# Kernel tuning notes

Hardware: AMD Instinct MI355X
Metric: run time of the kernel (lower is better)

Reference implementation:

```python
import jax, jax.numpy as jnp
import numpy as np

# Transformer_E (depth=1): Residual(PreNorm(MultiScaleRetention)) + Residual1(PreNorm1(FeedForward))
# MultiScaleRetention follows the standard RetNet parallel form, adapted to two inputs
# (Q from x, K/V from z) as implied by PreNorm passing both normed streams to fn.

B, S, DIM, HEADS, MLP = 16, 1024, 256, 4, 512
HEAD = DIM // HEADS  # per-head qkv size; v_dim = DIM
EPS = 1e-5           # torch LayerNorm/GroupNorm default eps


def _ln(x, w, b):
    mu = jnp.mean(x, -1, keepdims=True)
    var = jnp.mean((x - mu) ** 2, -1, keepdims=True)
    return (x - mu) * jax.lax.rsqrt(var + EPS) * w + b


def _decay_matrix():
    # RetNet gammas: 1 - exp(linspace(log(1/32), log(1/512), heads))
    gammas = 1.0 - jnp.exp(jnp.linspace(jnp.log(1.0 / 32.0), jnp.log(1.0 / 512.0), HEADS))
    n = jnp.arange(S)
    diff = (n[:, None] - n[None, :]).astype(jnp.float32)  # [S,S]
    causal = diff >= 0
    D = jnp.where(causal[None], gammas[:, None, None] ** diff[None], 0.0)  # [H,S,S]
    return D.astype(jnp.float32)


def setup_inputs() -> dict:
    key = jax.random.key(0)
    ks = jax.random.split(key, 9)
    s = 1.0 / DIM  # repo inits W as randn/hidden_size
    return {
        "x": jax.random.normal(ks[0], (B, S, DIM), jnp.float32),
        "y": jax.random.normal(ks[1], (B, S, DIM), jnp.float32),
        "ln1_w": jnp.ones((DIM,), jnp.float32),
        "ln1_b": jnp.zeros((DIM,), jnp.float32),
        "W_Q": jax.random.normal(ks[2], (HEADS, DIM, HEAD), jnp.float32) * s,
        "W_K": jax.random.normal(ks[3], (HEADS, DIM, HEAD), jnp.float32) * s,
        "W_V": jax.random.normal(ks[4], (HEADS, DIM, HEAD), jnp.float32) * s,
        "gn_w": jnp.ones((DIM,), jnp.float32),
        "gn_b": jnp.zeros((DIM,), jnp.float32),
        "W_G": jax.random.normal(ks[5], (DIM, DIM), jnp.float32) * s,
        "W_O": jax.random.normal(ks[6], (DIM, DIM), jnp.float32) * s,
        "ln2_w": jnp.ones((DIM,), jnp.float32),
        "ln2_b": jnp.zeros((DIM,), jnp.float32),
        "ff_w1": jax.random.normal(ks[7], (DIM, MLP), jnp.float32) * (DIM ** -0.5),
        "ff_b1": jnp.zeros((MLP,), jnp.float32),
        "ff_w2": jax.random.normal(ks[8], (MLP, DIM), jnp.float32) * (MLP ** -0.5),
        "ff_b2": jnp.zeros((DIM,), jnp.float32),
    }


def reference(x, y, ln1_w, ln1_b, W_Q, W_K, W_V, gn_w, gn_b, W_G, W_O,
              ln2_w, ln2_b, ff_w1, ff_b1, ff_w2, ff_b2):
    # PreNorm: x.real -> float (already real float32 here), shared LayerNorm on both streams
    xn = _ln(x, ln1_w, ln1_b)
    zn = _ln(y, ln1_w, ln1_b)

    # --- MultiScaleRetention (parallel form) ---
    Q = jnp.einsum('bsd,hde->bhse', xn, W_Q)
    K = jnp.einsum('bsd,hde->bhse', zn, W_K)
    V = jnp.einsum('bsd,hde->bhse', zn, W_V)
    D = _decay_matrix()                                       # [H,S,S] causal decay
    scores = jnp.einsum('bhne,bhme->bhnm', Q, K) * D[None]    # [B,H,S,S]
    Yh = jnp.einsum('bhnm,bhme->bhne', scores, V)             # [B,H,S,HEAD]

    # GroupNorm(heads, v_dim) applied token-wise: normalize each head slice
    mu = jnp.mean(Yh, -1, keepdims=True)
    var = jnp.mean((Yh - mu) ** 2, -1, keepdims=True)
    Yn = (Yh - mu) * jax.lax.rsqrt(var + EPS)
    Ycat = jnp.transpose(Yn, (0, 2, 1, 3)).reshape(x.shape[0], x.shape[1], DIM)
    Ycat = Ycat * gn_w + gn_b

    # swish gate + output projection
    g = xn @ W_G
    attn_out = ((g * jax.nn.sigmoid(g)) * Ycat) @ W_O

    x1 = attn_out + x                                         # Residual

    # --- FeedForward block (Residual1(PreNorm1(FFN))) ---
    x1n = _ln(x1, ln2_w, ln2_b)
    h = jax.nn.leaky_relu(x1n @ ff_w1 + ff_b1, negative_slope=0.01)
    ff = h @ ff_w2 + ff_b2
    return ff + x1
```

## Files before the change

kernel.cpp:

```cpp
#include <hip/hip_runtime.h>

typedef float f32x4 __attribute__((ext_vector_type(4)));
typedef short bf16x8 __attribute__((ext_vector_type(8)));

__device__ __forceinline__ unsigned short f2bf(float f) {
  unsigned int u = __builtin_bit_cast(unsigned int, f);
  u += 0x7fffu + ((u >> 16) & 1u);
  return (unsigned short)(u >> 16);
}
__device__ __forceinline__ float bf2f(unsigned short s) {
  unsigned int u = ((unsigned int)s) << 16;
  return __builtin_bit_cast(float, u);
}

__device__ __forceinline__ void gll16(const void* src, void* dst) {
  __builtin_amdgcn_global_load_lds((const __attribute__((address_space(1))) void*)src,
                                   (__attribute__((address_space(3))) void*)dst, 16, 0, 0);
}

__global__ __launch_bounds__(256) void prep(
    const float* __restrict__ x, const float* __restrict__ y,
    const float* __restrict__ ln1w, const float* __restrict__ ln1b,
    const float* __restrict__ WQ, const float* __restrict__ WK,
    const float* __restrict__ WV, const float* __restrict__ WG,
    const float* __restrict__ WO, const float* __restrict__ F1,
    const float* __restrict__ F2,
    unsigned short* __restrict__ XN, unsigned short* __restrict__ ZN,
    unsigned short* __restrict__ qg, unsigned short* __restrict__ kv,
    unsigned short* __restrict__ wo, unsigned short* __restrict__ f1,
    unsigned short* __restrict__ f2)
{
  __shared__ float tl[64 * 65];
  const int id = blockIdx.x;
  if (id < 8192) {
    const float* X = (id < 4096) ? x : y;
    unsigned short* Y = (id < 4096) ? XN : ZN;
    const int bid = id & 4095;
    const int lane = threadIdx.x & 63;
    const size_t row = (size_t)bid * 4 + (threadIdx.x >> 6);
    const float4 v = *reinterpret_cast<const float4*>(X + row * 256 + lane * 4);
    float s = v.x + v.y + v.z + v.w;
    #pragma unroll
    for (int off = 1; off < 64; off <<= 1) s += __shfl_xor(s, off);
    float mean = s * (1.0f / 256.0f);
    float dx = v.x - mean, dy = v.y - mean, dz = v.z - mean, dw = v.w - mean;
    float q = dx * dx + dy * dy + dz * dz + dw * dw;
    #pragma unroll
    for (int off = 1; off < 64; off <<= 1) q += __shfl_xor(q, off);
    float rstd = rsqrtf(q * (1.0f / 256.0f) + 1e-5f);
    float4 wv = *reinterpret_cast<const float4*>(ln1w + lane * 4);
    float4 bv = *reinterpret_cast<const float4*>(ln1b + lane * 4);
    ushort4 o;
    o.x = f2bf(dx * rstd * wv.x + bv.x);
    o.y = f2bf(dy * rstd * wv.y + bv.y);
    o.z = f2bf(dz * rstd * wv.z + bv.z);
    o.w = f2bf(dw * rstd * wv.w + bv.w);
    *reinterpret_cast<ushort4*>(Y + row * 256 + lane * 4) = o;
    return;
  }
  const int t = id - 8192;
  const float* srcp; unsigned short* dstp; int sstr, dstr;
  if (t < 48) {
    const float* W = (t < 16) ? WQ : (t < 32) ? WK : WV;
    unsigned short* D = (t < 16) ? qg : kv;
    int tt = t & 15, h = tt >> 2, dt = tt & 3;
    int nof = (t >= 32) ? 256 : 0;
    srcp = W + ((size_t)(h * 256 + dt * 64)) * 64; sstr = 64;
    dstp = D + ((size_t)(nof + h * 64)) * 256 + dt * 64; dstr = 256;
  } else if (t < 64) {
    int tt = t - 48, r = tt >> 2, cc = tt & 3;
    srcp = WG + (size_t)(r * 64) * 256 + cc * 64; sstr = 256;
    dstp = qg + (size_t)(256 + cc * 64) * 256 + r * 64; dstr = 256;
  } else if (t < 80) {
    int tt = t - 64, r = tt >> 2, cc = tt & 3;
    srcp = WO + (size_t)(r * 64) * 256 + cc * 64; sstr = 256;
    dstp = wo + (size_t)(cc * 64) * 256 + r * 64; dstr = 256;
  } else if (t < 112) {
    int tt = t - 80, r = tt >> 3, cc = tt & 7;
    srcp = F1 + (size_t)(r * 64) * 512 + cc * 64; sstr = 512;
    dstp = f1 + (size_t)(cc * 64) * 256 + r * 64; dstr = 256;
  } else {
    int tt = t - 112, r = tt >> 2, cc = tt & 3;
    srcp = F2 + (size_t)(r * 64) * 256 + cc * 64; sstr = 256;
    dstp = f2 + (size_t)(cc * 64) * 512 + r * 64; dstr = 512;
  }
  {
    const int row = threadIdx.x >> 2, cq = threadIdx.x & 3;
    #pragma unroll
    for (int q = 0; q < 4; ++q) {
      int col = cq * 16 + q * 4;
      float4 v = *reinterpret_cast<const float4*>(srcp + (size_t)row * sstr + col);
      tl[(col + 0) * 65 + row] = v.x;
      tl[(col + 1) * 65 + row] = v.y;
      tl[(col + 2) * 65 + row] = v.z;
      tl[(col + 3) * 65 + row] = v.w;
    }
    __syncthreads();
    const int c2 = threadIdx.x >> 2, kq = threadIdx.x & 3;
    bf16x8 v0, v1;
    #pragma unroll
    for (int k = 0; k < 8; ++k) {
      v0[k] = (short)f2bf(tl[c2 * 65 + kq * 16 + k]);
      v1[k] = (short)f2bf(tl[c2 * 65 + kq * 16 + 8 + k]);
    }
    *reinterpret_cast<bf16x8*>(dstp + (size_t)c2 * dstr + kq * 16) = v0;
    *reinterpret_cast<bf16x8*>(dstp + (size_t)c2 * dstr + kq * 16 + 8) = v1;
  }
}

template<int MODE>
__global__ __launch_bounds__(256) void gemm128(
    const unsigned short* __restrict__ A0, const unsigned short* __restrict__ A1,
    const unsigned short* __restrict__ B0, const unsigned short* __restrict__ B1,
    unsigned short* __restrict__ o0, unsigned short* __restrict__ o1,
    unsigned short* __restrict__ o2, unsigned short* __restrict__ o3,
    const float* __restrict__ bias)
{
  __shared__ __align__(16) char sA[2][16384];
  __shared__ __align__(16) char sB[2][16384];
  const int tid = threadIdx.x, lane = tid & 63, w = tid >> 6;
  const int z = (MODE == 0) ? blockIdx.z : 0;
  const unsigned short* A = (MODE == 0 && z) ? A1 : A0;
  const unsigned short* Bw = (MODE == 0 && z) ? B1 : B0;
  const int flat = blockIdx.x;
  const int c = flat & 7, jj = flat >> 3;
  const int m0 = (c * 16 + (jj & 15)) * 128;
  const int n0 = (jj >> 4) * 128;
  const int wr = (w >> 1) * 64, wc = (w & 1) * 64;
  const char* Ab = (const char*)A + (size_t)m0 * 512;
  const char* Bb = (const char*)Bw + (size_t)n0 * 512;
  const int srow = lane >> 3;
  const int soff = 16 * ((lane & 7) ^ srow);
  f32x4 acc[4][4] = {};

  auto stage = [&](int bufi, int kt) {
    #pragma unroll
    for (int p = 0; p < 4; ++p) {
      int row = p * 32 + w * 8 + srow;
      gll16(Ab + (size_t)row * 512 + kt + soff, &sA[bufi][p * 4096 + w * 1024]);
      gll16(Bb + (size_t)row * 512 + kt + soff, &sB[bufi][p * 4096 + w * 1024]);
    }
  };

  stage(0, 0);
  asm volatile("s_waitcnt vmcnt(0)" ::: "memory");
  __syncthreads();
  int buf = 0;
  for (int kt = 0; kt < 512; kt += 128) {
    if (kt + 128 < 512) stage(buf ^ 1, kt + 128);
    #pragma unroll
    for (int kk = 0; kk < 2; ++kk) {
      const int ib = kk * 64 + ((lane >> 4) * 16);
      bf16x8 af[4], bfr[4];
      #pragma unroll
      for (int rf = 0; rf < 4; ++rf) {
        int row = wr + rf * 16 + (lane & 15);
        af[rf] = *reinterpret_cast<const bf16x8*>(&sA[buf][row * 128 + (ib ^ ((row & 7) << 4))]);
      }
      #pragma unroll
      for (int cf = 0; cf < 4; ++cf) {
        int row = wc + cf * 16 + (lane & 15);
        bfr[cf] = *reinterpret_cast<const bf16x8*>(&sB[buf][row * 128 + (ib ^ ((row & 7) << 4))]);
      }
      #pragma unroll
      for (int rf = 0; rf < 4; ++rf)
        #pragma unroll
        for (int cf = 0; cf < 4; ++cf)
          acc[rf][cf] = __builtin_amdgcn_mfma_f32_16x16x32_bf16(af[rf], bfr[cf], acc[rf][cf], 0, 0, 0);
    }
    asm volatile("s_waitcnt vmcnt(0)" ::: "memory");
    __syncthreads();
    buf ^= 1;
  }

  if constexpr (MODE == 0) {
    if (z == 1 && n0 >= 256) {
      char* sT = (char*)sA;
      #pragma unroll
      for (int rf = 0; rf < 4; ++rf) {
        #pragma unroll
        for (int cf = 0; cf < 4; ++cf) {
          const int colL = wc + cf * 16 + (lane & 15);
          const int tokL = wr + rf * 16 + ((lane >> 4) * 4);
          f32x4 v = acc[rf][cf];
          #pragma unroll
          for (int j = 0; j < 4; ++j)
            *reinterpret_cast<unsigned short*>(
                sT + colL * 256 + (((tokL + j) * 2) ^ ((colL & 15) << 4))) = f2bf(v[j]);
        }
      }
      __syncthreads();
      const int b10 = m0 & 1023, bb = m0 >> 10;
      #pragma unroll
      for (int it = 0; it < 8; ++it) {
        int idx = it * 256 + tid, colL = idx >> 4, t16 = idx & 15;
        uint4 vv = *reinterpret_cast<uint4*>(sT + colL * 256 + ((t16 * 16) ^ ((colL & 15) << 4)));
        int vc = (n0 - 256) + colL, hh = vc >> 6, e = vc & 63;
        int bh = bb * 4 + hh;
        *reinterpret_cast<uint4*>(o3 + ((((size_t)bh * 64 + e) << 10) + b10 + t16 * 8)) = vv;
      }
      return;
    }
  }

  #pragma unroll
  for (int rf = 0; rf < 4; ++rf) {
    #pragma unroll
    for (int cf = 0; cf < 4; ++cf) {
      const int r0 = m0 + wr + rf * 16 + ((lane >> 4) * 4);
      const int col = n0 + wc + cf * 16 + (lane & 15);
      f32x4 v = acc[rf][cf];
      if constexpr (MODE == 1) {
        float bc = bias[col];
        #pragma unroll
        for (int j = 0; j < 4; ++j) {
          float t = v[j] + bc;
          o0[(size_t)(r0 + j) * 512 + col] = f2bf(t >= 0.0f ? t : 0.01f * t);
        }
      } else {
        if (z == 0) {
          const bool lowhalf = (n0 + wc + cf * 16) < 256;
          unsigned short* dst = lowhalf ? o0 : o1;
          int ccol = col & 255;
          #pragma unroll
          for (int j = 0; j < 4; ++j) dst[(size_t)(r0 + j) * 256 + ccol] = f2bf(v[j]);
        } else {
          #pragma unroll
          for (int j = 0; j < 4; ++j) o2[(size_t)(r0 + j) * 256 + col] = f2bf(v[j]);
        }
      }
    }
  }
}

template<int EPI>
__global__ __launch_bounds__(256) void gemm_nt(
    const unsigned short* __restrict__ A, const unsigned short* __restrict__ Bw,
    int K, unsigned short* __restrict__ o0,
    const float* __restrict__ bias, const float* __restrict__ resid,
    float* __restrict__ of)
{
  __shared__ __align__(16) char sA[2][16384];
  __shared__ __align__(16) char sB[2][8192];
  const int tid = threadIdx.x, lane = tid & 63, w = tid >> 6;
  const int flat = blockIdx.x + gridDim.x * blockIdx.y;
  const int c = flat & 7, jj = flat >> 3;
  const int m0 = (c * 16 + (jj & 15)) * 128;
  const int n0 = (jj >> 4) * 64;
  const int wr = (w >> 1) * 64, wc = (w & 1) * 32;
  const int K2 = K * 2;
  const char* Ab = (const char*)A + (size_t)m0 * K2;
  const char* Bb = (const char*)Bw + (size_t)n0 * K2;
  const int srow = lane >> 3;
  const int soff = 16 * ((lane & 7) ^ srow);
  f32x4 acc[4][2] = {};

  auto stage = [&](int bufi, int kt) {
    #pragma unroll
    for (int p = 0; p < 4; ++p) {
      int row = p * 32 + w * 8 + srow;
      gll16(Ab + (size_t)row * K2 + kt + soff, &sA[bufi][p * 4096 + w * 1024]);
    }
    #pragma unroll
    for (int p = 0; p < 2; ++p) {
      int row = p * 32 + w * 8 + srow;
      gll16(Bb + (size_t)row * K2 + kt + soff, &sB[bufi][p * 4096 + w * 1024]);
    }
  };

  stage(0, 0);
  asm volatile("s_waitcnt vmcnt(0)" ::: "memory");
  __syncthreads();
  int buf = 0;
  for (int kt = 0; kt < K2; kt += 128) {
    if (kt + 128 < K2) stage(buf ^ 1, kt + 128);
    #pragma unroll
    for (int kk = 0; kk < 2; ++kk) {
      const int ib = kk * 64 + ((lane >> 4) * 16);
      bf16x8 af[4], bfr[2];
      #pragma unroll
      for (int rf = 0; rf < 4; ++rf) {
        int row = wr + rf * 16 + (lane & 15);
        af[rf] = *reinterpret_cast<const bf16x8*>(&sA[buf][row * 128 + (ib ^ ((row & 7) << 4))]);
      }
      #pragma unroll
      for (int cf = 0; cf < 2; ++cf) {
        int row = wc + cf * 16 + (lane & 15);
        bfr[cf] = *reinterpret_cast<const bf16x8*>(&sB[buf][row * 128 + (ib ^ ((row & 7) << 4))]);
      }
      #pragma unroll
      for (int rf = 0; rf < 4; ++rf)
        #pragma unroll
        for (int cf = 0; cf < 2; ++cf)
          acc[rf][cf] = __builtin_amdgcn_mfma_f32_16x16x32_bf16(af[rf], bfr[cf], acc[rf][cf], 0, 0, 0);
    }
    asm volatile("s_waitcnt vmcnt(0)" ::: "memory");
    __syncthreads();
    buf ^= 1;
  }

  #pragma unroll
  for (int rf = 0; rf < 4; ++rf) {
    #pragma unroll
    for (int cf = 0; cf < 2; ++cf) {
      const int r0 = m0 + wr + rf * 16 + ((lane >> 4) * 4);
      const int col = n0 + wc + cf * 16 + (lane & 15);
      f32x4 v = acc[rf][cf];
      if constexpr (EPI == 3) {
        float bc = bias[col];
        #pragma unroll
        for (int j = 0; j < 4; ++j) {
          float t = v[j] + bc;
          o0[(size_t)(r0 + j) * 512 + col] = f2bf(t >= 0.0f ? t : 0.01f * t);
        }
      } else {
        float bc = bias[col];
        #pragma unroll
        for (int j = 0; j < 4; ++j) {
          size_t idx = (size_t)(r0 + j) * 256 + col;
          of[idx] = v[j] + bc + resid[idx];
        }
      }
    }
  }
}

__global__ __launch_bounds__(256) void gemm_wo_ln(
    const unsigned short* __restrict__ AY, const unsigned short* __restrict__ WoT,
    const float* __restrict__ x, const float* __restrict__ ln2w,
    const float* __restrict__ ln2b,
    float* __restrict__ X1, unsigned short* __restrict__ X1N)
{
  __shared__ __align__(16) char sA[2][4096];
  __shared__ __align__(16) char sB[2][32768];
  __shared__ float redS[32][4], redQ[32][4];
  const int tid = threadIdx.x, lane = tid & 63, w = tid >> 6;
  const int id = blockIdx.x;
  const int c = id & 7, j5 = id >> 3;
  const int m0 = (c * 64 + j5) * 32;
  const char* Ab = (const char*)AY + (size_t)m0 * 512;
  const char* Bb = (const char*)WoT;
  const int srow = lane >> 3;
  const int soff = 16 * ((lane & 7) ^ srow);
  f32x4 acc[2][4] = {};

  auto stage = [&](int bufi, int kt) {
    {
      int row = w * 8 + srow;
      gll16(Ab + (size_t)row * 512 + kt + soff, &sA[bufi][w * 1024]);
    }
    #pragma unroll
    for (int p = 0; p < 8; ++p) {
      int row = w * 64 + p * 8 + srow;
      gll16(Bb + (size_t)row * 512 + kt + soff, &sB[bufi][w * 8192 + p * 1024]);
    }
  };

  stage(0, 0);
  asm volatile("s_waitcnt vmcnt(0)" ::: "memory");
  __syncthreads();
  int buf = 0;
  for (int kt = 0; kt < 512; kt += 128) {
    if (kt + 128 < 512) stage(buf ^ 1, kt + 128);
    #pragma unroll
    for (int kk = 0; kk < 2; ++kk) {
      const int ib = kk * 64 + ((lane >> 4) * 16);
      bf16x8 af[2], bfr[4];
      #pragma unroll
      for (int mf = 0; mf < 2; ++mf) {
        int row = mf * 16 + (lane & 15);
        af[mf] = *reinterpret_cast<const bf16x8*>(&sA[buf][row * 128 + (ib ^ ((row & 7) << 4))]);
      }
      #pragma unroll
      for (int nf = 0; nf < 4; ++nf) {
        int row = w * 64 + nf * 16 + (lane & 15);
        bfr[nf] = *reinterpret_cast<const bf16x8*>(&sB[buf][row * 128 + (ib ^ ((row & 7) << 4))]);
      }
      #pragma unroll
      for (int mf = 0; mf < 2; ++mf)
        #pragma unroll
        for (int nf = 0; nf < 4; ++nf)
          acc[mf][nf] = __builtin_amdgcn_mfma_f32_16x16x32_bf16(af[mf], bfr[nf], acc[mf][nf], 0, 0, 0);
    }
    asm volatile("s_waitcnt vmcnt(0)" ::: "memory");
    __syncthreads();
    buf ^= 1;
  }

  #pragma unroll
  for (int mf = 0; mf < 2; ++mf) {
    #pragma unroll
    for (int j = 0; j < 4; ++j) {
      const int rowg = m0 + mf * 16 + ((lane >> 4) * 4) + j;
      float s = 0.0f, q = 0.0f;
      #pragma unroll
      for (int nf = 0; nf < 4; ++nf) {
        const int col = w * 64 + nf * 16 + (lane & 15);
        float v = acc[mf][nf][j] + x[(size_t)rowg * 256 + col];
        acc[mf][nf][j] = v;
        s += v; q += v * v;
      }
      #pragma unroll
      for (int off = 1; off < 16; off <<= 1) { s += __shfl_xor(s, off); q += __shfl_xor(q, off); }
      if ((lane & 15) == 0) {
        int rl = mf * 16 + ((lane >> 4) * 4) + j;
        redS[rl][w] = s; redQ[rl][w] = q;
      }
    }
  }
  __syncthreads();
  #pragma unroll
  for (int mf = 0; mf < 2; ++mf) {
    #pragma unroll
    for (int j = 0; j < 4; ++j) {
      const int rl = mf * 16 + ((lane >> 4) * 4) + j;
      const int rowg = m0 + rl;
      float sm = redS[rl][0] + redS[rl][1] + redS[rl][2] + redS[rl][3];
      float sq = redQ[rl][0] + redQ[rl][1] + redQ[rl][2] + redQ[rl][3];
      float mean = sm * (1.0f / 256.0f);
      float var = sq * (1.0f / 256.0f) - mean * mean;
      float rstd = rsqrtf(var + 1e-5f);
      #pragma unroll
      for (int nf = 0; nf < 4; ++nf) {
        const int col = w * 64 + nf * 16 + (lane & 15);
        float v = acc[mf][nf][j];
        X1[(size_t)rowg * 256 + col] = v;
        X1N[(size_t)rowg * 256 + col] = f2bf((v - mean) * rstd * ln2w[col] + ln2b[col]);
      }
    }
  }
}

__global__ __launch_bounds__(256) void attn_ret(
    const unsigned short* __restrict__ Qb, const unsigned short* __restrict__ Kb,
    const unsigned short* __restrict__ Vt, const unsigned short* __restrict__ Gb,
    const float* __restrict__ gnw, const float* __restrict__ gnb,
    unsigned short* __restrict__ AY)
{
  __shared__ __align__(16) char sK[2][8192];
  __shared__ __align__(16) char sV[2][8192];
  __shared__ __align__(16) char sP[8192];
  const int tid = threadIdx.x, lane = tid & 63, w = tid >> 6;
  const int id = blockIdx.x;
  const int c = id & 7, jid = id >> 3;
  const int bh = c * 8 + (jid & 7);
  const int g = jid >> 3;
  const int qt = (g < 4) ? (15 - g) : (g < 8) ? (11 - g) : (g < 12) ? g : (g - 12);
  const int b = bh >> 2, h = bh & 3;

  const float la = logf(1.0f / 32.0f), lb = logf(1.0f / 512.0f);
  const float gamma = 1.0f - expf(la + (lb - la) * ((float)h * (1.0f / 3.0f)));
  const float lg = log2f(gamma);

  const char* Qg = (const char*)Qb
      + ((size_t)(b * 1024 + qt * 64 + w * 16 + (lane & 15))) * 512 + h * 128 + (lane >> 4) * 16;
  const bf16x8 aq0 = *reinterpret_cast<const bf16x8*>(Qg);
  const bf16x8 aq1 = *reinterpret_cast<const bf16x8*>(Qg + 64);

  const int nloc_b = w * 16 + ((lane >> 4) * 4);
  float Aj[4], Bcf[4];
  #pragma unroll
  for (int j = 0; j < 4; ++j) Aj[j] = exp2f((float)(qt * 64 + nloc_b + j) * lg);
  #pragma unroll
  for (int cf = 0; cf < 4; ++cf) Bcf[cf] = exp2f(-(float)(cf * 16 + (lane & 15)) * lg);
  const float g64 = exp2f(-64.0f * lg);

  const char* Kg = (const char*)Kb + ((size_t)(b * 1024)) * 512 + h * 128;
  const char* Vg = (const char*)Vt + ((size_t)bh * 64) * 2048;
  const int srow = lane >> 3;
  const int soff = 16 * ((lane & 7) ^ srow);

  auto stage = [&](int bufi, int t) {
    const char* kb = Kg + (size_t)(t * 64) * 512;
    const char* vb = Vg + (size_t)(t * 64) * 2;
    #pragma unroll
    for (int p = 0; p < 2; ++p) {
      int row = p * 32 + w * 8 + srow;
      gll16(kb + (size_t)row * 512 + soff, &sK[bufi][p * 4096 + w * 1024]);
      gll16(vb + (size_t)row * 2048 + soff, &sV[bufi][p * 4096 + w * 1024]);
    }
  };

  stage(0, 0);
  f32x4 o[4] = {};
  asm volatile("s_waitcnt vmcnt(0)" ::: "memory");
  __syncthreads();
  int buf = 0;

  for (int t = 0; t <= qt; ++t) {
    if (t < qt) stage(buf ^ 1, t + 1);

    f32x4 s4[4] = {};
    #pragma unroll
    for (int kk = 0; kk < 2; ++kk) {
      const int ib = kk * 64 + ((lane >> 4) * 16);
      const bf16x8 aq = kk ? aq1 : aq0;
      #pragma unroll
      for (int cf = 0; cf < 4; ++cf) {
        int kr = cf * 16 + (lane & 15);
        bf16x8 bk = *reinterpret_cast<const bf16x8*>(&sK[buf][kr * 128 + (ib ^ ((kr & 7) << 4))]);
        s4[cf] = __builtin_amdgcn_mfma_f32_16x16x32_bf16(aq, bk, s4[cf], 0, 0, 0);
      }
    }

    const bool diag = (t == qt);
    #pragma unroll
    for (int cf = 0; cf < 4; ++cf) {
      const int mloc = cf * 16 + (lane & 15);
      #pragma unroll
      for (int j = 0; j < 4; ++j) {
        float p = s4[cf][j] * (Aj[j] * Bcf[cf]);
        if (diag && (nloc_b + j - mloc) < 0) p = 0.0f;
        int pr = nloc_b + j;
        *reinterpret_cast<unsigned short*>(sP + pr * 128 + ((mloc * 2) ^ ((pr & 7) << 4))) = f2bf(p);
      }
    }

    #pragma unroll
    for (int kk = 0; kk < 2; ++kk) {
      const int ib = kk * 64 + ((lane >> 4) * 16);
      int pr = w * 16 + (lane & 15);
      bf16x8 ap = *reinterpret_cast<const bf16x8*>(sP + pr * 128 + (ib ^ ((pr & 7) << 4)));
      #pragma unroll
      for (int cf = 0; cf < 4; ++cf) {
        int vr = cf * 16 + (lane & 15);
        bf16x8 bv = *reinterpret_cast<const bf16x8*>(&sV[buf][vr * 128 + (ib ^ ((vr & 7) << 4))]);
        o[cf] = __builtin_amdgcn_mfma_f32_16x16x32_bf16(ap, bv, o[cf], 0, 0, 0);
      }
    }
    #pragma unroll
    for (int j = 0; j < 4; ++j) Aj[j] *= g64;

    asm volatile("s_waitcnt vmcnt(0)" ::: "memory");
    __syncthreads();
    buf ^= 1;
  }

  float gw[4], gb[4];
  #pragma unroll
  for (int cf = 0; cf < 4; ++cf) {
    int col = h * 64 + cf * 16 + (lane & 15);
    gw[cf] = gnw[col]; gb[cf] = gnb[col];
  }
  const int tokb = b * 1024 + qt * 64 + nloc_b;
  #pragma unroll
  for (int j = 0; j < 4; ++j) {
    float sm = 0.0f, sq = 0.0f;
    #pragma unroll
    for (int cf = 0; cf < 4; ++cf) { float xv = o[cf][j]; sm += xv; sq += xv * xv; }
    #pragma unroll
    for (int off = 1; off < 16; off <<= 1) { sm += __shfl_xor(sm, off); sq += __shfl_xor(sq, off); }
    float mean = sm * (1.0f / 64.0f);
    float var = sq * (1.0f / 64.0f) - mean * mean;
    float rstd = rsqrtf(var + 1e-5f);
    size_t tok = (size_t)(tokb + j);
    #pragma unroll
    for (int cf = 0; cf < 4; ++cf) {
      int col = h * 64 + cf * 16 + (lane & 15);
      float yn = (o[cf][j] - mean) * rstd * gw[cf] + gb[cf];
      float gv = bf2f(Gb[tok * 256 + col]);
      float sg = gv / (1.0f + expf(-gv));
      AY[tok * 256 + col] = f2bf(yn * sg);
    }
  }
}

extern "C" void kernel_launch(void* const* d_in, const int* in_sizes, int n_in,
                              void* d_out, int out_size, void* d_ws, size_t ws_size,
                              hipStream_t stream) {
  const float* x     = (const float*)d_in[0];
  const float* y     = (const float*)d_in[1];
  const float* ln1_w = (const float*)d_in[2];
  const float* ln1_b = (const float*)d_in[3];
  const float* W_Q   = (const float*)d_in[4];
  const float* W_K   = (const float*)d_in[5];
  const float* W_V   = (const float*)d_in[6];
  const float* gn_w  = (const float*)d_in[7];
  const float* gn_b  = (const float*)d_in[8];
  const float* W_G   = (const float*)d_in[9];
  const float* W_O   = (const float*)d_in[10];
  const float* ln2_w = (const float*)d_in[11];
  const float* ln2_b = (const float*)d_in[12];
  const float* ff_w1 = (const float*)d_in[13];
  const float* ff_b1 = (const float*)d_in[14];
  const float* ff_w2 = (const float*)d_in[15];
  const float* ff_b2 = (const float*)d_in[16];

  char* ws = (char*)d_ws;
  const size_t MB = 1048576;
  unsigned short* XN  = (unsigned short*)(ws + 0 * MB);
  unsigned short* ZN  = (unsigned short*)(ws + 8 * MB);
  unsigned short* QB  = (unsigned short*)(ws + 16 * MB);
  unsigned short* KB  = (unsigned short*)(ws + 24 * MB);
  unsigned short* VT  = (unsigned short*)(ws + 32 * MB);
  unsigned short* GB  = (unsigned short*)(ws + 40 * MB);
  unsigned short* WQG = (unsigned short*)(ws + 48 * MB);
  unsigned short* WKV = (unsigned short*)(ws + 48 * MB + 262144);
  unsigned short* WOp = (unsigned short*)(ws + 48 * MB + 524288);
  unsigned short* F1p = (unsigned short*)(ws + 48 * MB + 655360);
  unsigned short* F2p = (unsigned short*)(ws + 48 * MB + 917504);
  float*          X1  = (float*)(ws + 16 * MB);
  unsigned short* X1N = (unsigned short*)(ws + 32 * MB);
  unsigned short* H   = (unsigned short*)(ws + 0 * MB);
  unsigned short* AY  = ZN;
  float* out = (float*)d_out;

  prep<<<8336, 256, 0, stream>>>(x, y, ln1_w, ln1_b, W_Q, W_K, W_V, W_G, W_O,
                                 ff_w1, ff_w2, XN, ZN, WQG, WKV, WOp, F1p, F2p);
  gemm128<0><<<dim3(512, 1, 2), 256, 0, stream>>>(XN, ZN, WQG, WKV, QB, GB, KB, VT, nullptr);
  attn_ret<<<1024, 256, 0, stream>>>(QB, KB, VT, GB, gn_w, gn_b, AY);
  gemm_wo_ln<<<512, 256, 0, stream>>>(AY, WOp, x, ln2_w, ln2_b, X1, X1N);
  gemm128<1><<<dim3(512, 1, 1), 256, 0, stream>>>(X1N, nullptr, F1p, nullptr, H, nullptr, nullptr, nullptr, ff_b1);
  gemm_nt<4><<<dim3(4, 128), 256, 0, stream>>>(H, F2p, 512, nullptr, ff_b2, X1, out);
}
```

Measured before the change: 94.31 us.

## Use 128-row query tiles in retention kernel and 128x128 tiles for FFN2 GEMM

The retention kernel now gives each block 128 query rows across 8 waves (512 threads), so every staged K/V tile is shared by twice as many query rows. Waves skip key tiles that lie entirely above their causal diagonal. The second FFN GEMM moves from the 128x64 gemm_nt kernel to the 128x128 gemm128 template with a new bias+residual epilogue, which halves the number of blocks. The trade-off is higher per-block register and LDS use and coarser load balance across CUs.

```diff
diff --git a/kernel.cpp b/kernel.cpp
--- a/kernel.cpp
+++ b/kernel.cpp
@@ -114,8 +114,10 @@
     const unsigned short* __restrict__ B0, const unsigned short* __restrict__ B1,
     unsigned short* __restrict__ o0, unsigned short* __restrict__ o1,
     unsigned short* __restrict__ o2, unsigned short* __restrict__ o3,
-    const float* __restrict__ bias)
+    const float* __restrict__ bias, const float* __restrict__ resid,
+    float* __restrict__ of)
 {
+  constexpr int KB2 = (MODE == 2) ? 1024 : 512;
   __shared__ __align__(16) char sA[2][16384];
   __shared__ __align__(16) char sB[2][16384];
   const int tid = threadIdx.x, lane = tid & 63, w = tid >> 6;
@@ -127,8 +129,8 @@
   const int m0 = (c * 16 + (jj & 15)) * 128;
   const int n0 = (jj >> 4) * 128;
   const int wr = (w >> 1) * 64, wc = (w & 1) * 64;
-  const char* Ab = (const char*)A + (size_t)m0 * 512;
-  const char* Bb = (const char*)Bw + (size_t)n0 * 512;
+  const char* Ab = (const char*)A + (size_t)m0 * KB2;
+  const char* Bb = (const char*)Bw + (size_t)n0 * KB2;
   const int srow = lane >> 3;
   const int soff = 16 * ((lane & 7) ^ srow);
   f32x4 acc[4][4] = {};
@@ -137,8 +139,8 @@
     #pragma unroll
     for (int p = 0; p < 4; ++p) {
       int row = p * 32 + w * 8 + srow;
-      gll16(Ab + (size_t)row * 512 + kt + soff, &sA[bufi][p * 4096 + w * 1024]);
-      gll16(Bb + (size_t)row * 512 + kt + soff, &sB[bufi][p * 4096 + w * 1024]);
+      gll16(Ab + (size_t)row * KB2 + kt + soff, &sA[bufi][p * 4096 + w * 1024]);
+      gll16(Bb + (size_t)row * KB2 + kt + soff, &sB[bufi][p * 4096 + w * 1024]);
     }
   };
 
@@ -146,8 +148,8 @@
   asm volatile("s_waitcnt vmcnt(0)" ::: "memory");
   __syncthreads();
   int buf = 0;
-  for (int kt = 0; kt < 512; kt += 128) {
-    if (kt + 128 < 512) stage(buf ^ 1, kt + 128);
+  for (int kt = 0; kt < KB2; kt += 128) {
+    if (kt + 128 < KB2) stage(buf ^ 1, kt + 128);
     #pragma unroll
     for (int kk = 0; kk < 2; ++kk) {
       const int ib = kk * 64 + ((lane >> 4) * 16);
@@ -216,6 +218,13 @@
         for (int j = 0; j < 4; ++j) {
           float t = v[j] + bc;
           o0[(size_t)(r0 + j) * 512 + col] = f2bf(t >= 0.0f ? t : 0.01f * t);
+        }
+      } else if constexpr (MODE == 2) {
+        float bc = bias[col];
+        #pragma unroll
+        for (int j = 0; j < 4; ++j) {
+          size_t idx = (size_t)(r0 + j) * 256 + col;
+          of[idx] = v[j] + bc + resid[idx];
         }
       } else {
         if (z == 0) {
@@ -227,98 +236,6 @@
         } else {
           #pragma unroll
           for (int j = 0; j < 4; ++j) o2[(size_t)(r0 + j) * 256 + col] = f2bf(v[j]);
-        }
-      }
-    }
-  }
-}
-
-template<int EPI>
-__global__ __launch_bounds__(256) void gemm_nt(
-    const unsigned short* __restrict__ A, const unsigned short* __restrict__ Bw,
-    int K, unsigned short* __restrict__ o0,
-    const float* __restrict__ bias, const float* __restrict__ resid,
-    float* __restrict__ of)
-{
-  __shared__ __align__(16) char sA[2][16384];
-  __shared__ __align__(16) char sB[2][8192];
-  const int tid = threadIdx.x, lane = tid & 63, w = tid >> 6;
-  const int flat = blockIdx.x + gridDim.x * blockIdx.y;
-  const int c = flat & 7, jj = flat >> 3;
-  const int m0 = (c * 16 + (jj & 15)) * 128;
-  const int n0 = (jj >> 4) * 64;
-  const int wr = (w >> 1) * 64, wc = (w & 1) * 32;
-  const int K2 = K * 2;
-  const char* Ab = (const char*)A + (size_t)m0 * K2;
-  const char* Bb = (const char*)Bw + (size_t)n0 * K2;
-  const int srow = lane >> 3;
-  const int soff = 16 * ((lane & 7) ^ srow);
-  f32x4 acc[4][2] = {};
-
-  auto stage = [&](int bufi, int kt) {
-    #pragma unroll
-    for (int p = 0; p < 4; ++p) {
-      int row = p * 32 + w * 8 + srow;
-      gll16(Ab + (size_t)row * K2 + kt + soff, &sA[bufi][p * 4096 + w * 1024]);
-    }
-    #pragma unroll
-    for (int p = 0; p < 2; ++p) {
-      int row = p * 32 + w * 8 + srow;
-      gll16(Bb + (size_t)row * K2 + kt + soff, &sB[bufi][p * 4096 + w * 1024]);
-    }
-  };
-
-  stage(0, 0);
-  asm volatile("s_waitcnt vmcnt(0)" ::: "memory");
-  __syncthreads();
-  int buf = 0;
-  for (int kt = 0; kt < K2; kt += 128) {
-    if (kt + 128 < K2) stage(buf ^ 1, kt + 128);
-    #pragma unroll
-    for (int kk = 0; kk < 2; ++kk) {
-      const int ib = kk * 64 + ((lane >> 4) * 16);
-      bf16x8 af[4], bfr[2];
-      #pragma unroll
-      for (int rf = 0; rf < 4; ++rf) {
-        int row = wr + rf * 16 + (lane & 15);
-        af[rf] = *reinterpret_cast<const bf16x8*>(&sA[buf][row * 128 + (ib ^ ((row & 7) << 4))]);
-      }
-      #pragma unroll
-      for (int cf = 0; cf < 2; ++cf) {
-        int row = wc + cf * 16 + (lane & 15);
-        bfr[cf] = *reinterpret_cast<const bf16x8*>(&sB[buf][row * 128 + (ib ^ ((row & 7) << 4))]);
-      }
-      #pragma unroll
-      for (int rf = 0; rf < 4; ++rf)
-        #pragma unroll
-        for (int cf = 0; cf < 2; ++cf)
-          acc[rf][cf] = __builtin_amdgcn_mfma_f32_16x16x32_bf16(af[rf], bfr[cf], acc[rf][cf], 0, 0, 0);
-    }
-    asm volatile("s_waitcnt vmcnt(0)" ::: "memory");
-    __syncthreads();
-    buf ^= 1;
-  }
-
-  #pragma unroll
-  for (int rf = 0; rf < 4; ++rf) {
-    #pragma unroll
-    for (int cf = 0; cf < 2; ++cf) {
-      const int r0 = m0 + wr + rf * 16 + ((lane >> 4) * 4);
-      const int col = n0 + wc + cf * 16 + (lane & 15);
-      f32x4 v = acc[rf][cf];
-      if constexpr (EPI == 3) {
-        float bc = bias[col];
-        #pragma unroll
-        for (int j = 0; j < 4; ++j) {
-          float t = v[j] + bc;
-          o0[(size_t)(r0 + j) * 512 + col] = f2bf(t >= 0.0f ? t : 0.01f * t);
-        }
-      } else {
-        float bc = bias[col];
-        #pragma unroll
-        for (int j = 0; j < 4; ++j) {
-          size_t idx = (size_t)(r0 + j) * 256 + col;
-          of[idx] = v[j] + bc + resid[idx];
         }
       }
     }
@@ -431,7 +348,7 @@
   }
 }
 
-__global__ __launch_bounds__(256) void attn_ret(
+__global__ __launch_bounds__(512) void attn_ret8(
     const unsigned short* __restrict__ Qb, const unsigned short* __restrict__ Kb,
     const unsigned short* __restrict__ Vt, const unsigned short* __restrict__ Gb,
     const float* __restrict__ gnw, const float* __restrict__ gnb,
@@ -439,13 +356,13 @@
 {
   __shared__ __align__(16) char sK[2][8192];
   __shared__ __align__(16) char sV[2][8192];
-  __shared__ __align__(16) char sP[8192];
+  __shared__ __align__(16) char sP[16384];
   const int tid = threadIdx.x, lane = tid & 63, w = tid >> 6;
   const int id = blockIdx.x;
-  const int c = id & 7, jid = id >> 3;
-  const int bh = c * 8 + (jid & 7);
-  const int g = jid >> 3;
-  const int qt = (g < 4) ? (15 - g) : (g < 8) ? (11 - g) : (g < 12) ? g : (g - 12);
+  const int c = id & 7, bh = c * 8 + ((id >> 3) & 7);
+  const int qg = id >> 6;
+  const int perm[8] = {7, 4, 6, 5, 0, 3, 1, 2};
+  const int qt2 = perm[qg];
   const int b = bh >> 2, h = bh & 3;
 
   const float la = logf(1.0f / 32.0f), lb = logf(1.0f / 512.0f);
@@ -453,14 +370,15 @@
   const float lg = log2f(gamma);
 
   const char* Qg = (const char*)Qb
-      + ((size_t)(b * 1024 + qt * 64 + w * 16 + (lane & 15))) * 512 + h * 128 + (lane >> 4) * 16;
+      + ((size_t)(b * 1024 + qt2 * 128 + w * 16 + (lane & 15))) * 512 + h * 128 + (lane >> 4) * 16;
   const bf16x8 aq0 = *reinterpret_cast<const bf16x8*>(Qg);
   const bf16x8 aq1 = *reinterpret_cast<const bf16x8*>(Qg + 64);
 
   const int nloc_b = w * 16 + ((lane >> 4) * 4);
+  const int qlo = qt2 * 128 + w * 16;
   float Aj[4], Bcf[4];
   #pragma unroll
-  for (int j = 0; j < 4; ++j) Aj[j] = exp2f((float)(qt * 64 + nloc_b + j) * lg);
+  for (int j = 0; j < 4; ++j) Aj[j] = exp2f((float)(qt2 * 128 + nloc_b + j) * lg);
   #pragma unroll
   for (int cf = 0; cf < 4; ++cf) Bcf[cf] = exp2f(-(float)(cf * 16 + (lane & 15)) * lg);
   const float g64 = exp2f(-64.0f * lg);
@@ -473,12 +391,9 @@
   auto stage = [&](int bufi, int t) {
     const char* kb = Kg + (size_t)(t * 64) * 512;
     const char* vb = Vg + (size_t)(t * 64) * 2;
-    #pragma unroll
-    for (int p = 0; p < 2; ++p) {
-      int row = p * 32 + w * 8 + srow;
-      gll16(kb + (size_t)row * 512 + soff, &sK[bufi][p * 4096 + w * 1024]);
-      gll16(vb + (size_t)row * 2048 + soff, &sV[bufi][p * 4096 + w * 1024]);
-    }
+    int row = w * 8 + srow;
+    gll16(kb + (size_t)row * 512 + soff, &sK[bufi][w * 1024]);
+    gll16(vb + (size_t)row * 2048 + soff, &sV[bufi][w * 1024]);
   };
 
   stage(0, 0);
@@ -487,45 +402,50 @@
   __syncthreads();
   int buf = 0;
 
-  for (int t = 0; t <= qt; ++t) {
-    if (t < qt) stage(buf ^ 1, t + 1);
-
-    f32x4 s4[4] = {};
-    #pragma unroll
-    for (int kk = 0; kk < 2; ++kk) {
-      const int ib = kk * 64 + ((lane >> 4) * 16);
-      const bf16x8 aq = kk ? aq1 : aq0;
+  const int lt = 2 * qt2 + 1;
+  for (int t = 0; t <= lt; ++t) {
+    if (t < lt) stage(buf ^ 1, t + 1);
+
+    const int mrel = t * 64;
+    const bool skip = (mrel > qlo + 15);
+    if (!skip) {
+      f32x4 s4[4] = {};
+      #pragma unroll
+      for (int kk = 0; kk < 2; ++kk) {
+        const int ib = kk * 64 + ((lane >> 4) * 16);
+        const bf16x8 aq = kk ? aq1 : aq0;
+        #pragma unroll
+        for (int cf = 0; cf < 4; ++cf) {
+          int kr = cf * 16 + (lane & 15);
+          bf16x8 bk = *reinterpret_cast<const bf16x8*>(&sK[buf][kr * 128 + (ib ^ ((kr & 7) << 4))]);
+          s4[cf] = __builtin_amdgcn_mfma_f32_16x16x32_bf16(aq, bk, s4[cf], 0, 0, 0);
+        }
+      }
+
+      const bool full = (mrel + 63 <= qlo);
       #pragma unroll
       for (int cf = 0; cf < 4; ++cf) {
-        int kr = cf * 16 + (lane & 15);
-        bf16x8 bk = *reinterpret_cast<const bf16x8*>(&sK[buf][kr * 128 + (ib ^ ((kr & 7) << 4))]);
-        s4[cf] = __builtin_amdgcn_mfma_f32_16x16x32_bf16(aq, bk, s4[cf], 0, 0, 0);
-      }
-    }
-
-    const bool diag = (t == qt);
-    #pragma unroll
-    for (int cf = 0; cf < 4; ++cf) {
-      const int mloc = cf * 16 + (lane & 15);
-      #pragma unroll
-      for (int j = 0; j < 4; ++j) {
-        float p = s4[cf][j] * (Aj[j] * Bcf[cf]);
-        if (diag && (nloc_b + j - mloc) < 0) p = 0.0f;
-        int pr = nloc_b + j;
-        *reinterpret_cast<unsigned short*>(sP + pr * 128 + ((mloc * 2) ^ ((pr & 7) << 4))) = f2bf(p);
-      }
-    }
-
-    #pragma unroll
-    for (int kk = 0; kk < 2; ++kk) {
-      const int ib = kk * 64 + ((lane >> 4) * 16);
-      int pr = w * 16 + (lane & 15);
-      bf16x8 ap = *reinterpret_cast<const bf16x8*>(sP + pr * 128 + (ib ^ ((pr & 7) << 4)));
-      #pragma unroll
-      for (int cf = 0; cf < 4; ++cf) {
-        int vr = cf * 16 + (lane & 15);
-        bf16x8 bv = *reinterpret_cast<const bf16x8*>(&sV[buf][vr * 128 + (ib ^ ((vr & 7) << 4))]);
-        o[cf] = __builtin_amdgcn_mfma_f32_16x16x32_bf16(ap, bv, o[cf], 0, 0, 0);
+        const int mloc = cf * 16 + (lane & 15);
+        #pragma unroll
+        for (int j = 0; j < 4; ++j) {
+          float p = s4[cf][j] * (Aj[j] * Bcf[cf]);
+          if (!full && (qt2 * 128 + nloc_b + j - mrel - mloc) < 0) p = 0.0f;
+          int pr = nloc_b + j;
+          *reinterpret_cast<unsigned short*>(sP + pr * 128 + ((mloc * 2) ^ ((pr & 7) << 4))) = f2bf(p);
+        }
+      }
+
+      #pragma unroll
+      for (int kk = 0; kk < 2; ++kk) {
+        const int ib = kk * 64 + ((lane >> 4) * 16);
+        int pr = w * 16 + (lane & 15);
+        bf16x8 ap = *reinterpret_cast<const bf16x8*>(sP + pr * 128 + (ib ^ ((pr & 7) << 4)));
+        #pragma unroll
+        for (int cf = 0; cf < 4; ++cf) {
+          int vr = cf * 16 + (lane & 15);
+          bf16x8 bv = *reinterpret_cast<const bf16x8*>(&sV[buf][vr * 128 + (ib ^ ((vr & 7) << 4))]);
+          o[cf] = __builtin_amdgcn_mfma_f32_16x16x32_bf16(ap, bv, o[cf], 0, 0, 0);
+        }
       }
     }
     #pragma unroll
@@ -542,7 +462,7 @@
     int col = h * 64 + cf * 16 + (lane & 15);
     gw[cf] = gnw[col]; gb[cf] = gnb[col];
   }
-  const int tokb = b * 1024 + qt * 64 + nloc_b;
+  const int tokb = b * 1024 + qt2 * 128 + nloc_b;
   #pragma unroll
   for (int j = 0; j < 4; ++j) {
     float sm = 0.0f, sq = 0.0f;
@@ -607,9 +527,12 @@
 
   prep<<<8336, 256, 0, stream>>>(x, y, ln1_w, ln1_b, W_Q, W_K, W_V, W_G, W_O,
                                  ff_w1, ff_w2, XN, ZN, WQG, WKV, WOp, F1p, F2p);
-  gemm128<0><<<dim3(512, 1, 2), 256, 0, stream>>>(XN, ZN, WQG, WKV, QB, GB, KB, VT, nullptr);
-  attn_ret<<<1024, 256, 0, stream>>>(QB, KB, VT, GB, gn_w, gn_b, AY);
+  gemm128<0><<<dim3(512, 1, 2), 256, 0, stream>>>(XN, ZN, WQG, WKV, QB, GB, KB, VT,
+                                                  nullptr, nullptr, nullptr);
+  attn_ret8<<<512, 512, 0, stream>>>(QB, KB, VT, GB, gn_w, gn_b, AY);
   gemm_wo_ln<<<512, 256, 0, stream>>>(AY, WOp, x, ln2_w, ln2_b, X1, X1N);
-  gemm128<1><<<dim3(512, 1, 1), 256, 0, stream>>>(X1N, nullptr, F1p, nullptr, H, nullptr, nullptr, nullptr, ff_b1);
-  gemm_nt<4><<<dim3(4, 128), 256, 0, stream>>>(H, F2p, 512, nullptr, ff_b2, X1, out);
-}
+  gemm128<1><<<dim3(512, 1, 1), 256, 0, stream>>>(X1N, nullptr, F1p, nullptr, H, nullptr,
+                                                  nullptr, nullptr, ff_b1, nullptr, nullptr);
+  gemm128<2><<<dim3(256, 1, 1), 256, 0, stream>>>(H, nullptr, F2p, nullptr, nullptr, nullptr,
+                                                  nullptr, nullptr, ff_b2, X1, out);
+}
```

Result: slower. 108.0 us (+14.5%).

## Load K/V fragments directly from global memory instead of LDS staging

Applied to the files above, without the earlier changes.

Drops the double-buffered LDS staging of K and V tiles in the retention kernel, along with the per-tile barrier and wait. Each wave now reads its MFMA B-operand fragments straight from global memory. The aim is to remove barrier and LDS round-trip overhead and to cut LDS usage, which may raise occupancy. In exchange, all four waves fetch the same K/V data redundantly through the cache, and there is no explicit prefetch to hide global load latency.

```diff
diff --git a/kernel.cpp b/kernel.cpp
--- a/kernel.cpp
+++ b/kernel.cpp
@@ -437,8 +437,6 @@
     const float* __restrict__ gnw, const float* __restrict__ gnb,
     unsigned short* __restrict__ AY)
 {
-  __shared__ __align__(16) char sK[2][8192];
-  __shared__ __align__(16) char sV[2][8192];
   __shared__ __align__(16) char sP[8192];
   const int tid = threadIdx.x, lane = tid & 63, w = tid >> 6;
   const int id = blockIdx.x;
@@ -465,40 +463,22 @@
   for (int cf = 0; cf < 4; ++cf) Bcf[cf] = exp2f(-(float)(cf * 16 + (lane & 15)) * lg);
   const float g64 = exp2f(-64.0f * lg);
 
-  const char* Kg = (const char*)Kb + ((size_t)(b * 1024)) * 512 + h * 128;
-  const char* Vg = (const char*)Vt + ((size_t)bh * 64) * 2048;
-  const int srow = lane >> 3;
-  const int soff = 16 * ((lane & 7) ^ srow);
-
-  auto stage = [&](int bufi, int t) {
-    const char* kb = Kg + (size_t)(t * 64) * 512;
-    const char* vb = Vg + (size_t)(t * 64) * 2;
-    #pragma unroll
-    for (int p = 0; p < 2; ++p) {
-      int row = p * 32 + w * 8 + srow;
-      gll16(kb + (size_t)row * 512 + soff, &sK[bufi][p * 4096 + w * 1024]);
-      gll16(vb + (size_t)row * 2048 + soff, &sV[bufi][p * 4096 + w * 1024]);
-    }
-  };
-
-  stage(0, 0);
+  const char* Kbase = (const char*)Kb
+      + ((size_t)(b * 1024 + (lane & 15))) * 512 + h * 128 + (lane >> 4) * 16;
+  const char* Vbase = (const char*)Vt
+      + ((size_t)(bh * 64 + (lane & 15))) * 2048 + (lane >> 4) * 16;
+
   f32x4 o[4] = {};
-  asm volatile("s_waitcnt vmcnt(0)" ::: "memory");
-  __syncthreads();
-  int buf = 0;
 
   for (int t = 0; t <= qt; ++t) {
-    if (t < qt) stage(buf ^ 1, t + 1);
-
     f32x4 s4[4] = {};
     #pragma unroll
     for (int kk = 0; kk < 2; ++kk) {
-      const int ib = kk * 64 + ((lane >> 4) * 16);
       const bf16x8 aq = kk ? aq1 : aq0;
       #pragma unroll
       for (int cf = 0; cf < 4; ++cf) {
-        int kr = cf * 16 + (lane & 15);
-        bf16x8 bk = *reinterpret_cast<const bf16x8*>(&sK[buf][kr * 128 + (ib ^ ((kr & 7) << 4))]);
+        const bf16x8 bk = *reinterpret_cast<const bf16x8*>(
+            Kbase + (size_t)(t * 64 + cf * 16) * 512 + kk * 64);
         s4[cf] = __builtin_amdgcn_mfma_f32_16x16x32_bf16(aq, bk, s4[cf], 0, 0, 0);
       }
     }
@@ -523,17 +503,13 @@
       bf16x8 ap = *reinterpret_cast<const bf16x8*>(sP + pr * 128 + (ib ^ ((pr & 7) << 4)));
       #pragma unroll
       for (int cf = 0; cf < 4; ++cf) {
-        int vr = cf * 16 + (lane & 15);
-        bf16x8 bv = *reinterpret_cast<const bf16x8*>(&sV[buf][vr * 128 + (ib ^ ((vr & 7) << 4))]);
+        const bf16x8 bv = *reinterpret_cast<const bf16x8*>(
+            Vbase + (size_t)(cf * 16) * 2048 + t * 128 + kk * 64);
         o[cf] = __builtin_amdgcn_mfma_f32_16x16x32_bf16(ap, bv, o[cf], 0, 0, 0);
       }
     }
     #pragma unroll
     for (int j = 0; j < 4; ++j) Aj[j] *= g64;
-
-    asm volatile("s_waitcnt vmcnt(0)" ::: "memory");
-    __syncthreads();
-    buf ^= 1;
   }
 
   float gw[4], gb[4];
```

Measured after the change: 140.5 us. 49.0% more time.
